# Performance work log

Hardware: AMD Instinct MI355X
Metric: run time of the kernel (lower is better)

Reference implementation:

```python
import jax, jax.numpy as jnp
import numpy as np

B, NI, NO = 32, 64, 64


def setup_inputs() -> dict:
    key = jax.random.key(0)
    k1, k2, k3, k4, k5, k6 = jax.random.split(key, 6)
    return {
        "input_re": jax.random.normal(k1, (B, NI, NI), dtype=jnp.float32),
        "input_im": jax.random.normal(k2, (B, NI, NI), dtype=jnp.float32),
        "w_re": jax.random.normal(k3, (NI, NI, NO, NO), dtype=jnp.float32),
        "w_im": jax.random.normal(k4, (NI, NI, NO, NO), dtype=jnp.float32),
        "amp_weights": jax.random.normal(k5, (NI, NI), dtype=jnp.float32),
        "phase_weights": jax.random.normal(k6, (NI, NI), dtype=jnp.float32),
    }


def reference(input_re, input_im, w_re, w_im, amp_weights, phase_weights):
    # complex input field (B, NI, NI) and diffraction kernel (NI, NI, NO, NO)
    e_in = jax.lax.complex(input_re, input_im)
    w_ip = jax.lax.complex(w_re, w_im)
    # passive transmission coefficients: sigmoid(amp) * exp(i*phase)
    ts = (jax.nn.sigmoid(amp_weights)
          * jnp.exp(1j * phase_weights.astype(jnp.complex64))).astype(jnp.complex64)
    # modulated field, then sum over input pixels (i,j) -> complex GEMM
    modulated = e_in * ts[None, :, :]                    # (B, NI, NI)
    out = jnp.einsum('bij,ijkl->bkl', modulated, w_ip)   # (B, NO, NO)
    return out
```

## Files before the change

kernel.cpp:

```cpp
#include <hip/hip_runtime.h>
#include <cstdint>
#include <cstddef>

#define KC 4096
#define NN 4096
#define NB 32
#define HALF (NB * NN)

typedef __attribute__((ext_vector_type(8))) short  bf16x8;
typedef __attribute__((ext_vector_type(16))) float f32x16;

__device__ __forceinline__ unsigned short f2bf(float f) {
    union { float f; unsigned u; } v; v.f = f;
    unsigned r = v.u + 0x7fffu + ((v.u >> 16) & 1u);
    return (unsigned short)(r >> 16);
}

__global__ __launch_bounds__(256) void prep_kernel(
    const float* __restrict__ in_re, const float* __restrict__ in_im,
    const float* __restrict__ amp,   const float* __restrict__ phase,
    uint32_t* __restrict__ wsA)
{
    int tid = blockIdx.x * 256 + threadIdx.x;
    int b = tid >> 12;
    int k = tid & (KC - 1);
    float er = in_re[tid], ei = in_im[tid];
    float a = amp[k], p = phase[k];
    float s = 1.0f / (1.0f + expf(-a));
    float sn, cs;
    sincosf(p, &sn, &cs);
    float tr = s * cs, ti = s * sn;
    float mr = er * tr - ei * ti;
    float mi = er * ti + ei * tr;
    uint32_t pk = (uint32_t)f2bf(mr) | ((uint32_t)f2bf(mi) << 16);
    wsA[((((k >> 2) << 5) + b) << 2) | (k & 3)] = pk;
}

__global__ __launch_bounds__(256) void gemm_kernel(
    const float* __restrict__ w_re, const float* __restrict__ w_im,
    const bf16x8* __restrict__ wsA, float2* __restrict__ wsP, int steps)
{
    const int lane = threadIdx.x & 63;
    const int wave = threadIdx.x >> 6;
    const int h    = lane >> 5;
    const int l32  = lane & 31;
    const int n    = blockIdx.x * 128 + wave * 32 + l32;
    const int s    = blockIdx.y;
    const int kbase = s * (steps * 8);

    f32x16 accR = {};
    f32x16 accI = {};

    const bf16x8* aptr = wsA + ((size_t)(kbase >> 2) + h) * 32 + l32;
    const float* pre = w_re + (size_t)(kbase + h * 4) * NN + n;
    const float* pim = w_im + (size_t)(kbase + h * 4) * NN + n;

#pragma unroll 4
    for (int t = 0; t < steps; ++t) {
        bf16x8 afrag = aptr[(size_t)(2 * t) * 32];
        const float* pr = pre + (size_t)t * 8 * NN;
        const float* pi = pim + (size_t)t * 8 * NN;
        float r0 = pr[0], r1 = pr[NN], r2 = pr[2 * NN], r3 = pr[3 * NN];
        float i0 = pi[0], i1 = pi[NN], i2 = pi[2 * NN], i3 = pi[3 * NN];

        bf16x8 bR, bI;
        bR[0] = (short)f2bf(r0);  bR[1] = (short)f2bf(-i0);
        bR[2] = (short)f2bf(r1);  bR[3] = (short)f2bf(-i1);
        bR[4] = (short)f2bf(r2);  bR[5] = (short)f2bf(-i2);
        bR[6] = (short)f2bf(r3);  bR[7] = (short)f2bf(-i3);
        bI[0] = (short)f2bf(i0);  bI[1] = (short)f2bf(r0);
        bI[2] = (short)f2bf(i1);  bI[3] = (short)f2bf(r1);
        bI[4] = (short)f2bf(i2);  bI[5] = (short)f2bf(r2);
        bI[6] = (short)f2bf(i3);  bI[7] = (short)f2bf(r3);

        accR = __builtin_amdgcn_mfma_f32_32x32x16_bf16(afrag, bR, accR, 0, 0, 0);
        accI = __builtin_amdgcn_mfma_f32_32x32x16_bf16(afrag, bI, accI, 0, 0, 0);
    }

#pragma unroll
    for (int r = 0; r < 16; ++r) {
        int brow = (r & 3) + 8 * (r >> 2) + 4 * h;
        float2 v; v.x = accR[r]; v.y = accI[r];
        wsP[((size_t)s * NB + brow) * NN + n] = v;
    }
}

__global__ __launch_bounds__(256) void reduce_kernel(
    const float2* __restrict__ wsP, float* __restrict__ out, int S)
{
    int tid = blockIdx.x * 256 + threadIdx.x;
    float re = 0.f, im = 0.f;
    for (int s = 0; s < S; ++s) {
        float2 v = wsP[(size_t)s * (NB * NN) + tid];
        re += v.x; im += v.y;
    }
    out[tid]        = re;
    out[HALF + tid] = im;
}

extern "C" void kernel_launch(void* const* d_in, const int* in_sizes, int n_in,
                              void* d_out, int out_size, void* d_ws, size_t ws_size,
                              hipStream_t stream)
{
    const float* in_re  = (const float*)d_in[0];
    const float* in_im  = (const float*)d_in[1];
    const float* w_re   = (const float*)d_in[2];
    const float* w_im   = (const float*)d_in[3];
    const float* amp    = (const float*)d_in[4];
    const float* phase  = (const float*)d_in[5];

    const size_t A_BYTES = (size_t)1024 * 32 * 16;
    uint32_t* wsA = (uint32_t*)d_ws;
    float2*   wsP = (float2*)((char*)d_ws + A_BYTES);

    int S = 16;
    while (S > 1 && A_BYTES + (size_t)S * NB * NN * sizeof(float2) > ws_size) S >>= 1;
    int steps = (KC / S) / 8;

    prep_kernel<<<dim3((NB * KC) / 256), dim3(256), 0, stream>>>(
        in_re, in_im, amp, phase, wsA);

    gemm_kernel<<<dim3(NN / 128, S), dim3(256), 0, stream>>>(
        w_re, w_im, (const bf16x8*)wsA, wsP, steps);

    reduce_kernel<<<dim3((NB * NN) / 256), dim3(256), 0, stream>>>(
        wsP, (float*)d_out, S);
}
```

Baseline: 166.9 us.

## Software-pipeline weight loads in GEMM, pack bf16 pairs directly, double split-K

Restructures the GEMM main loop to prefetch the next step's A fragment and eight weight floats while converting and multiplying the current step. The B fragments are now built by packing bf16 pairs into 32-bit words, with the sign flip done by an XOR instead of a separate conversion of the negated value. The split-K factor is raised from 16 to 32 to launch more blocks for the memory-bound weight stream, and launch bounds request 4 blocks per CU. In exchange the reduce kernel reads twice as many partial sums, and the prefetch raises register pressure.

```diff
diff --git a/kernel.cpp b/kernel.cpp
--- a/kernel.cpp
+++ b/kernel.cpp
@@ -10,10 +10,10 @@
 typedef __attribute__((ext_vector_type(8))) short  bf16x8;
 typedef __attribute__((ext_vector_type(16))) float f32x16;
 
-__device__ __forceinline__ unsigned short f2bf(float f) {
+__device__ __forceinline__ uint32_t f2bf(float f) {
     union { float f; unsigned u; } v; v.f = f;
     unsigned r = v.u + 0x7fffu + ((v.u >> 16) & 1u);
-    return (unsigned short)(r >> 16);
+    return r >> 16;
 }
 
 __global__ __launch_bounds__(256) void prep_kernel(
@@ -32,11 +32,11 @@
     float tr = s * cs, ti = s * sn;
     float mr = er * tr - ei * ti;
     float mi = er * ti + ei * tr;
-    uint32_t pk = (uint32_t)f2bf(mr) | ((uint32_t)f2bf(mi) << 16);
+    uint32_t pk = f2bf(mr) | (f2bf(mi) << 16);
     wsA[((((k >> 2) << 5) + b) << 2) | (k & 3)] = pk;
 }
 
-__global__ __launch_bounds__(256) void gemm_kernel(
+__global__ __launch_bounds__(256, 4) void gemm_kernel(
     const float* __restrict__ w_re, const float* __restrict__ w_im,
     const bf16x8* __restrict__ wsA, float2* __restrict__ wsP, int steps)
 {
@@ -55,26 +55,42 @@
     const float* pre = w_re + (size_t)(kbase + h * 4) * NN + n;
     const float* pim = w_im + (size_t)(kbase + h * 4) * NN + n;
 
-#pragma unroll 4
-    for (int t = 0; t < steps; ++t) {
-        bf16x8 afrag = aptr[(size_t)(2 * t) * 32];
-        const float* pr = pre + (size_t)t * 8 * NN;
-        const float* pi = pim + (size_t)t * 8 * NN;
-        float r0 = pr[0], r1 = pr[NN], r2 = pr[2 * NN], r3 = pr[3 * NN];
-        float i0 = pi[0], i1 = pi[NN], i2 = pi[2 * NN], i3 = pi[3 * NN];
+    bf16x8 af = aptr[0];
+    float r0 = pre[0], r1 = pre[NN], r2 = pre[2 * NN], r3 = pre[3 * NN];
+    float i0 = pim[0], i1 = pim[NN], i2 = pim[2 * NN], i3 = pim[3 * NN];
 
-        bf16x8 bR, bI;
-        bR[0] = (short)f2bf(r0);  bR[1] = (short)f2bf(-i0);
-        bR[2] = (short)f2bf(r1);  bR[3] = (short)f2bf(-i1);
-        bR[4] = (short)f2bf(r2);  bR[5] = (short)f2bf(-i2);
-        bR[6] = (short)f2bf(r3);  bR[7] = (short)f2bf(-i3);
-        bI[0] = (short)f2bf(i0);  bI[1] = (short)f2bf(r0);
-        bI[2] = (short)f2bf(i1);  bI[3] = (short)f2bf(r1);
-        bI[4] = (short)f2bf(i2);  bI[5] = (short)f2bf(r2);
-        bI[6] = (short)f2bf(i3);  bI[7] = (short)f2bf(r3);
+    for (int t = 0; t < steps - 1; ++t) {
+        bf16x8 afn = aptr[(size_t)(2 * (t + 1)) * 32];
+        const float* prn = pre + (size_t)(t + 1) * 8 * NN;
+        const float* pin = pim + (size_t)(t + 1) * 8 * NN;
+        float r0n = prn[0], r1n = prn[NN], r2n = prn[2 * NN], r3n = prn[3 * NN];
+        float i0n = pin[0], i1n = pin[NN], i2n = pin[2 * NN], i3n = pin[3 * NN];
 
-        accR = __builtin_amdgcn_mfma_f32_32x32x16_bf16(afrag, bR, accR, 0, 0, 0);
-        accI = __builtin_amdgcn_mfma_f32_32x32x16_bf16(afrag, bI, accI, 0, 0, 0);
+        uint32_t R0 = f2bf(r0), R1 = f2bf(r1), R2 = f2bf(r2), R3 = f2bf(r3);
+        uint32_t I0 = f2bf(i0), I1 = f2bf(i1), I2 = f2bf(i2), I3 = f2bf(i3);
+        union { bf16x8 v; uint32_t d[4]; } uR, uI;
+        uR.d[0] = R0 | ((I0 ^ 0x8000u) << 16);  uI.d[0] = I0 | (R0 << 16);
+        uR.d[1] = R1 | ((I1 ^ 0x8000u) << 16);  uI.d[1] = I1 | (R1 << 16);
+        uR.d[2] = R2 | ((I2 ^ 0x8000u) << 16);  uI.d[2] = I2 | (R2 << 16);
+        uR.d[3] = R3 | ((I3 ^ 0x8000u) << 16);  uI.d[3] = I3 | (R3 << 16);
+        accR = __builtin_amdgcn_mfma_f32_32x32x16_bf16(af, uR.v, accR, 0, 0, 0);
+        accI = __builtin_amdgcn_mfma_f32_32x32x16_bf16(af, uI.v, accI, 0, 0, 0);
+
+        af = afn;
+        r0 = r0n; r1 = r1n; r2 = r2n; r3 = r3n;
+        i0 = i0n; i1 = i1n; i2 = i2n; i3 = i3n;
+    }
+
+    {
+        uint32_t R0 = f2bf(r0), R1 = f2bf(r1), R2 = f2bf(r2), R3 = f2bf(r3);
+        uint32_t I0 = f2bf(i0), I1 = f2bf(i1), I2 = f2bf(i2), I3 = f2bf(i3);
+        union { bf16x8 v; uint32_t d[4]; } uR, uI;
+        uR.d[0] = R0 | ((I0 ^ 0x8000u) << 16);  uI.d[0] = I0 | (R0 << 16);
+        uR.d[1] = R1 | ((I1 ^ 0x8000u) << 16);  uI.d[1] = I1 | (R1 << 16);
+        uR.d[2] = R2 | ((I2 ^ 0x8000u) << 16);  uI.d[2] = I2 | (R2 << 16);
+        uR.d[3] = R3 | ((I3 ^ 0x8000u) << 16);  uI.d[3] = I3 | (R3 << 16);
+        accR = __builtin_amdgcn_mfma_f32_32x32x16_bf16(af, uR.v, accR, 0, 0, 0);
+        accI = __builtin_amdgcn_mfma_f32_32x32x16_bf16(af, uI.v, accI, 0, 0, 0);
     }
 
 #pragma unroll
@@ -113,7 +129,7 @@
     uint32_t* wsA = (uint32_t*)d_ws;
     float2*   wsP = (float2*)((char*)d_ws + A_BYTES);
 
-    int S = 16;
+    int S = 32;
     while (S > 1 && A_BYTES + (size_t)S * NB * NN * sizeof(float2) > ws_size) S >>= 1;
     int steps = (KC / S) / 8;
 
```

Result: slower. 174.0 us (+4.2%).
